# Optimization experiments

Hardware: AMD Instinct MI355X
Metric: run time of the kernel (lower is better)

The kernel has to match this reference:

```python
import jax, jax.numpy as jnp
import numpy as np
from jax.scipy.special import gammaln

# sizes (see shape_source)
N_CELLS = 1024
N_GENES = 1000
N_LATENT = 50
NB_ENC = 16          # encoder histogram bins per gene
NB_DEC = 16          # decoder mixture components (sum(n_decoder_bins))
N_HID = 16           # encoder hidden dim
N_CUTS = 4_000_000
N_FRAGS = 2_000_000
N_TOTAL_CELLS = 10_000
N_TOTAL_CUTS = 50_000_000
BN_EPS = 1e-5


def _normal_logprob(x, loc, scale):
    z = (x - loc) / scale
    return -0.5 * z * z - jnp.log(scale) - 0.5 * jnp.log(2.0 * jnp.pi)


def setup_inputs() -> dict:
    key = jax.random.key(0)
    ks = jax.random.split(key, 20)
    cut_coordinates = jax.random.uniform(ks[0], (N_CUTS,), dtype=jnp.float32)
    cut_cell = jax.random.randint(ks[1], (N_CUTS,), 0, N_CELLS)
    cut_local_gene_ix = jax.random.randint(ks[2], (N_CUTS,), 0, N_GENES)
    cut_local_cellxgene_ix = cut_cell * N_GENES + cut_local_gene_ix
    local_cellxgene_ix = jax.random.randint(ks[3], (N_FRAGS,), 0, N_CELLS * N_GENES)
    genes_oi = jnp.arange(N_GENES)
    cells_oi = jnp.arange(N_CELLS)
    eps = jax.random.normal(ks[4], (N_CELLS, N_LATENT), dtype=jnp.float32)
    n_in = N_GENES * NB_ENC
    enc_W1 = jax.random.normal(ks[5], (n_in, N_HID)) * (1.0 / np.sqrt(n_in))
    enc_b1 = jnp.zeros((N_HID,))
    bn_gamma = jnp.ones((N_HID,))
    bn_beta = jnp.zeros((N_HID,))
    W_loc = jax.random.normal(ks[6], (N_HID, N_LATENT)) * (1.0 / np.sqrt(N_HID))
    b_loc = jnp.zeros((N_LATENT,))
    W_scale = jax.random.normal(ks[7], (N_HID, N_LATENT)) * (1.0 / np.sqrt(N_HID))
    b_scale = jnp.zeros((N_LATENT,))
    logit_weight = jax.random.normal(ks[8], (N_GENES, N_LATENT, NB_DEC)) * 0.05
    rho_weight = jax.random.normal(ks[9], (N_GENES, N_LATENT)) * 0.05
    baseline_heights = jax.random.normal(ks[10], (N_GENES, NB_DEC)) * 0.1
    libsize = jax.random.randint(ks[11], (N_TOTAL_CELLS,), 1000, 20000)
    rho_bias = jax.random.uniform(ks[12], (N_GENES,), minval=1e-4, maxval=1e-2)
    return dict(
        cut_coordinates=cut_coordinates, eps=eps,
        enc_W1=enc_W1, enc_b1=enc_b1, bn_gamma=bn_gamma, bn_beta=bn_beta,
        W_loc=W_loc, b_loc=b_loc, W_scale=W_scale, b_scale=b_scale,
        logit_weight=logit_weight, rho_weight=rho_weight,
        baseline_heights=baseline_heights, rho_bias=rho_bias,
        cut_local_cellxgene_ix=cut_local_cellxgene_ix,
        cut_local_gene_ix=cut_local_gene_ix,
        local_cellxgene_ix=local_cellxgene_ix,
        genes_oi=genes_oi, cells_oi=cells_oi, libsize=libsize,
    )


def reference(cut_coordinates, eps, enc_W1, enc_b1, bn_gamma, bn_beta,
              W_loc, b_loc, W_scale, b_scale, logit_weight, rho_weight,
              baseline_heights, rho_bias, cut_local_cellxgene_ix,
              cut_local_gene_ix, local_cellxgene_ix, genes_oi, cells_oi,
              libsize):
    n_cells = cells_oi.shape[0]
    n_genes = genes_oi.shape[0]

    # ---- Encoder: digitize + bincount histogram ----
    bin_enc = jnp.minimum(jnp.floor(cut_coordinates * NB_ENC), NB_ENC - 1).astype(jnp.int32)
    digitized = bin_enc + cut_local_cellxgene_ix.astype(jnp.int32) * NB_ENC
    counts = jax.ops.segment_sum(jnp.ones_like(cut_coordinates), digitized,
                                 num_segments=n_cells * n_genes * NB_ENC)
    x = jnp.log1p(counts.reshape(n_cells, n_genes * NB_ENC))  # [C, G*NB]

    h = x @ enc_W1 + enc_b1
    mu = h.mean(axis=0)
    var = h.var(axis=0)  # biased, matches torch BN in train mode
    h = (h - mu) / jnp.sqrt(var + BN_EPS) * bn_gamma + bn_beta
    h = jax.nn.relu(h)
    loc = h @ W_loc + b_loc                 # [C, L]
    scale = jnp.exp(h @ W_scale + b_scale)  # [C, L]

    # ---- latent sample + KL ----
    q_scale = scale * 0.1
    latent = loc + q_scale * eps
    latent_kl = (_normal_logprob(latent, 0.0, 1.0)
                 - _normal_logprob(latent, loc, q_scale)) * (N_TOTAL_CELLS / n_cells)

    # ---- Decoder (n_layers=0: per-gene linear heads) ----
    lw = logit_weight[genes_oi]                       # [G, L, K]
    rw = rho_weight[genes_oi]                         # [G, L]
    mixture_delta = jnp.einsum('cl,glk->cgk', latent, lw)  # [C, G, K]
    rho_delta = jnp.einsum('cl,gl->cg', latent, rw)        # [C, G]
    md_cxg = mixture_delta.reshape(n_cells * n_genes, NB_DEC)
    md_cut = md_cxg[cut_local_cellxgene_ix]           # [N_CUTS, K] gather
    mixture_delta_kl = _normal_logprob(lw, 0.0, 0.1)

    # ---- mixture likelihood: piecewise-constant spline density per cut ----
    logits = baseline_heights[cut_local_gene_ix] + md_cut  # [N_CUTS, K]
    logp = jax.nn.log_softmax(logits, axis=-1)
    bin_dec = jnp.minimum(jnp.floor(cut_coordinates * NB_DEC), NB_DEC - 1).astype(jnp.int32)
    likelihood_mixture = (jnp.take_along_axis(logp, bin_dec[:, None], axis=1)[:, 0]
                          + jnp.log(float(NB_DEC)))

    # ---- fragment-count Poisson likelihood ----
    fragexpr = (rho_bias[genes_oi][None, :] * jnp.exp(rho_delta)
                * libsize[cells_oi].astype(jnp.float32)[:, None])  # [C, G]
    fragmentcounts = jax.ops.segment_sum(
        jnp.ones((local_cellxgene_ix.shape[0],), jnp.float32),
        local_cellxgene_ix, num_segments=n_cells * n_genes
    ).reshape(n_cells, n_genes)
    likelihood_frag = (fragmentcounts * jnp.log(fragexpr) - fragexpr
                       - gammaln(fragmentcounts + 1.0))

    rho_delta_kl = _normal_logprob(rw, 0.0, 0.1)

    likelihood = (likelihood_mixture.sum() * (N_TOTAL_CUTS / cut_coordinates.shape[0])
                  + likelihood_frag.sum() * (N_TOTAL_CELLS / n_cells))
    elbo = (-likelihood - latent_kl.sum() - mixture_delta_kl.sum()
            - rho_delta_kl.sum())
    return elbo
```

## Files before the change

kernel.cpp:

```cpp
#include <hip/hip_runtime.h>
#include <hip/hip_bf16.h>
#include <math.h>


#define G_      1000
#define C_      1024
#define L_      50
#define K_      16
#define NHID_   16
#define CUT_SCALE   12.5f
#define CELL_SCALE  9.765625f

#define CHUNK_    6144
#define RCAP_CUT  18432
#define RCAP_FRAG 9216

#define GCNTC_OFF  0ull
#define GCNTF_OFF  1024ull
#define DONE_OFF   2048ull
#define DACC_OFF   6400ull
#define HT_OFF     6912ull
#define ZERO_BYTES 72448ull
#define LATBF_OFF  72448ull
#define LWT_OFF    203520ull
#define ENTC_OFF   2251520ull
#define ENTF_OFF   11688704ull
#define MERGED_OFF 16407296ull
#define FRAGU8_OFF 24599296ull
#define LATT_OFF   25623296ull
#define WS_NEED    25828096ull

typedef __attribute__((ext_vector_type(8))) short short8;
typedef __attribute__((ext_vector_type(4))) float f32x4;

__device__ __constant__ float LGT[32] = {
    0.0f, 0.0f, 0.6931471805599453f, 1.791759469228055f, 3.1780538303479458f,
    4.787491742782046f, 6.579251212010101f, 8.525161361065415f,
    10.60460290274525f, 12.801827480081469f, 15.104412573075516f,
    17.502307845873887f, 19.987214495661885f, 22.552163853123425f,
    25.19122118273868f, 27.89927138384089f, 30.671860106080672f,
    33.50507345013689f, 36.39544520803305f, 39.339884187199495f,
    42.335616460753485f, 45.38013889847691f, 48.47118135183523f,
    51.60667556776438f, 54.78472939811232f, 58.00360522298052f,
    61.261701761002f, 64.55753862700633f, 67.88974313718154f,
    71.25703896716801f, 74.65823634883016f, 78.0922235533153f };

__device__ __forceinline__ double atomAddF64(double* p, double v) {
    return __hip_atomic_fetch_add(p, v, __ATOMIC_RELAXED,
                                  __HIP_MEMORY_SCOPE_AGENT);
}

__device__ __forceinline__ float block_sum_256(float v) {
    __shared__ float sm[256];
    int t = threadIdx.x;
    __syncthreads();
    sm[t] = v;
    __syncthreads();
#pragma unroll
    for (int s = 128; s > 0; s >>= 1) {
        if (t < s) sm[t] += sm[t + s];
        __syncthreads();
    }
    return sm[0];
}

__global__ __launch_bounds__(256)
void part_kernel(const int* __restrict__ cut_ix,
                 const float* __restrict__ coord,
                 const int* __restrict__ frag_ix,
                 unsigned int* __restrict__ gcnt_c,
                 unsigned int* __restrict__ gcnt_f,
                 unsigned short* __restrict__ entc,
                 unsigned short* __restrict__ entf,
                 const float* __restrict__ lw,
                 const float* __restrict__ rw,
                 __hip_bfloat16* __restrict__ lwT,
                 double* __restrict__ dacc,
                 int n_cuts, int n_frags, int ncc, int nblk_part) {
    int t = threadIdx.x;
    int bid = blockIdx.x;
    if (bid >= nblk_part) {
        int r = bid - nblk_part;
        if (r < 256) {
            for (int g = r; g < G_; g += 256) {
                for (int i = t; i < L_ * K_; i += 256) {
                    float v = lw[(size_t)g * (L_ * K_) + i];
                    lwT[(size_t)g * 1024 + (i & 15) * 64 + (i >> 4)] =
                        __float2bfloat16(v);
                }
                for (int i = t; i < 16 * 14; i += 256) {
                    int n = i / 14, l = 50 + (i % 14);
                    lwT[(size_t)g * 1024 + n * 64 + l] = __float2bfloat16(0.f);
                }
            }
        } else {
            const int NTOT = G_ * L_ * K_ + G_ * L_;
            int wb = r - 256;
            float s = 0.f;
            for (int i = wb * 256 + t; i < NTOT; i += 256 * 256) {
                float w = (i < G_ * L_ * K_) ? lw[i] : rw[i - G_ * L_ * K_];
                s += fmaf(-50.f * w, w, 1.3836465597893733f);
            }
            s = block_sum_256(s);
            if (t == 0) atomAddF64(&dacc[wb & 63], (double)(-s));
        }
        return;
    }
    __shared__ unsigned int cnt[256], excl[256], cur[256], gbas[256];
    __shared__ unsigned short stage[CHUNK_];
    __shared__ unsigned char bkof[CHUNK_];
    bool isCut = (bid < ncc);
    int blk = isCut ? bid : bid - ncc;
    const int* idx = isCut ? cut_ix : frag_ix;
    int n = isCut ? n_cuts : n_frags;
    int rcap = isCut ? RCAP_CUT : RCAP_FRAG;
    unsigned int* gcount = isCut ? gcnt_c : gcnt_f;
    unsigned short* ent = isCut ? entc : entf;
    int i0 = blk * CHUNK_;
    cnt[t] = 0;
    int4 I[6]; float4 X[6];
    unsigned int vm;
    bool full = (i0 + CHUNK_ <= n);
    if (full) {
        const int4* ip = (const int4*)(idx + i0);
#pragma unroll
        for (int k = 0; k < 6; ++k) I[k] = ip[k * 256 + t];
        if (isCut) {
            const float4* xp = (const float4*)(coord + i0);
#pragma unroll
            for (int k = 0; k < 6; ++k) X[k] = xp[k * 256 + t];
        }
        vm = 0xFFFFFFu;
    } else {
        vm = 0;
#pragma unroll
        for (int k = 0; k < 6; ++k) {
            int r0 = i0 + (k * 256 + t) * 4;
            int* Ii = (int*)&I[k]; float* Xi = (float*)&X[k];
#pragma unroll
            for (int u = 0; u < 4; ++u) {
                bool v = (r0 + u) < n;
                if (v) vm |= 1u << (k * 4 + u);
                Ii[u] = v ? idx[r0 + u] : 0;
                Xi[u] = (v && isCut) ? coord[r0 + u] : 0.f;
            }
        }
    }
    __syncthreads();
#pragma unroll
    for (int k = 0; k < 6; ++k) {
        const int* Ii = (const int*)&I[k];
        const float* Xi = (const float*)&X[k];
#pragma unroll
        for (int u = 0; u < 4; ++u) {
            if (vm & (1u << (k * 4 + u))) {
                int ix = Ii[u];
                int c = ix / G_;
                int g = ix - c * G_;
                unsigned int bk;
                if (isCut) {
                    int b = (int)(Xi[u] * 16.f); b = b > 15 ? 15 : b;
                    bk = ((unsigned)(c >> 6) << 4) | ((unsigned)(g * K_ + b) >> 10);
                } else {
                    bk = ((unsigned)(c >> 6) << 4) | ((unsigned)g >> 6);
                }
                atomicAdd(&cnt[bk], 1u);
            }
        }
    }
    __syncthreads();
    if (t < 64) {
        unsigned int c0 = cnt[t * 4 + 0], c1 = cnt[t * 4 + 1];
        unsigned int c2 = cnt[t * 4 + 2], c3 = cnt[t * 4 + 3];
        unsigned int tot = c0 + c1 + c2 + c3;
        unsigned int run = tot;
#pragma unroll
        for (int o = 1; o < 64; o <<= 1) {
            unsigned int v = __shfl_up(run, o, 64);
            if (t >= o) run += v;
        }
        unsigned int base = run - tot;
        excl[t * 4 + 0] = base;
        excl[t * 4 + 1] = base + c0;
        excl[t * 4 + 2] = base + c0 + c1;
        excl[t * 4 + 3] = base + c0 + c1 + c2;
    }
    __syncthreads();
    gbas[t] = cnt[t] ? atomicAdd(&gcount[t], cnt[t]) : 0u;
    cur[t] = excl[t];
    __syncthreads();
#pragma unroll
    for (int k = 0; k < 6; ++k) {
        const int* Ii = (const int*)&I[k];
        const float* Xi = (const float*)&X[k];
#pragma unroll
        for (int u = 0; u < 4; ++u) {
            if (vm & (1u << (k * 4 + u))) {
                int ix = Ii[u];
                int c = ix / G_;
                int g = ix - c * G_;
                unsigned int bk; unsigned short e;
                if (isCut) {
                    int b = (int)(Xi[u] * 16.f); b = b > 15 ? 15 : b;
                    int bin = g * K_ + b;
                    bk = ((unsigned)(c >> 6) << 4) | ((unsigned)bin >> 10);
                    e = (unsigned short)(((c & 63) << 10) | (bin & 1023));
                } else {
                    bk = ((unsigned)(c >> 6) << 4) | ((unsigned)g >> 6);
                    e = (unsigned short)(((c & 63) << 6) | (g & 63));
                }
                unsigned int p = atomicAdd(&cur[bk], 1u);
                stage[p] = e;
                bkof[p] = (unsigned char)bk;
            }
        }
    }
    __syncthreads();
    int total = n - i0; if (total > CHUNK_) total = CHUNK_;
    for (int p = t; p < total; p += 256) {
        unsigned int bk = bkof[p];
        unsigned int dst = gbas[bk] + (p - excl[bk]);
        if (dst < (unsigned)rcap)
            ent[(size_t)bk * rcap + dst] = stage[p];
    }
}

__global__ __launch_bounds__(256)
void mid_kernel(const unsigned int* __restrict__ gcnt_c,
                const unsigned short* __restrict__ entc,
                const unsigned int* __restrict__ gcnt_f,
                const unsigned short* __restrict__ entf,
                const float* __restrict__ W1,
                unsigned int* __restrict__ merged,
                unsigned int* __restrict__ fragw,
                float* __restrict__ hT) {
    __shared__ unsigned int h[4096];
    __shared__ float w1s[4096];
    int t = threadIdx.x;
    int bid = blockIdx.x;
    if (bid < 512) {
        int bk = bid >> 1, half = bid & 1;
        int cg = bk >> 4, bc = bk & 15;
        for (int i = t; i < 4096; i += 256) h[i] = 0;
        __syncthreads();
        unsigned int count = gcnt_c[bk];
        if (count > RCAP_CUT) count = RCAP_CUT;
        const unsigned int* e32 = (const unsigned int*)(entc + (size_t)bk * RCAP_CUT);
        unsigned int hsel = (unsigned)half << 5;
        unsigned int npair = count >> 1;
        for (unsigned int base = 0; base < npair; base += 1024) {
            unsigned int w[4]; bool val[4];
#pragma unroll
            for (int u = 0; u < 4; ++u) {
                unsigned int p = base + u * 256 + t;
                val[u] = (p < npair);
                w[u] = val[u] ? e32[p] : 0u;
            }
#pragma unroll
            for (int u = 0; u < 4; ++u) {
                if (val[u]) {
                    unsigned int v0 = w[u] & 0xffffu, v1 = w[u] >> 16;
                    unsigned int c0 = v0 >> 10, c1 = v1 >> 10;
                    if ((c0 & 32u) == hsel) {
                        unsigned int cc = c0 & 31u;
                        atomicAdd(&h[(v0 & 1023u) * 4 + (cc >> 3)],
                                  1u << ((cc & 7) * 4));
                    }
                    if ((c1 & 32u) == hsel) {
                        unsigned int cc = c1 & 31u;
                        atomicAdd(&h[(v1 & 1023u) * 4 + (cc >> 3)],
                                  1u << ((cc & 7) * 4));
                    }
                }
            }
        }
        if (t == 0 && (count & 1u)) {
            unsigned int v = ((const unsigned short*)e32)[count - 1];
            unsigned int c0 = v >> 10;
            if ((c0 & 32u) == hsel) {
                unsigned int cc = c0 & 31u;
                atomicAdd(&h[(v & 1023u) * 4 + (cc >> 3)], 1u << ((cc & 7) * 4));
            }
        }
        __syncthreads();
        for (int i = t; i < 4096; i += 256) {
            int binlo = i >> 2, wq = i & 3;
            int bin = bc * 1024 + binlo;
            if (bin < 16000)
                merged[(unsigned)bin * 128u + (unsigned)(cg * 8 + half * 4 + wq)]
                    = h[i];
        }
        int c32 = t & 31, sub = t >> 5;
        int sh = (c32 & 7) * 4, widx = c32 >> 3;
        float acc[NHID_];
#pragma unroll
        for (int j = 0; j < NHID_; ++j) acc[j] = 0.f;
        for (int q = 0; q < 4; ++q) {
            __syncthreads();
            int wbase = (bc * 1024 + q * 256) * NHID_;
#pragma unroll
            for (int r = 0; r < 16; ++r) {
                int i = r * 256 + t;
                int gi = wbase + i;
                w1s[i] = (gi < 16000 * NHID_) ? W1[gi] : 0.f;
            }
            __syncthreads();
            const float4* w1v = (const float4*)w1s;
            int rl0 = q * 256 + sub * 32;
#pragma unroll 4
            for (int bl = 0; bl < 32; ++bl) {
                int rl = rl0 + bl;
                int rwc = sub * 32 + bl;
                unsigned int w = h[rl * 4 + widx];
                float xv = __logf((float)(((w >> sh) & 0xfu) + 1u));
                float4 wa = w1v[rwc * 4 + 0];
                float4 wb = w1v[rwc * 4 + 1];
                float4 wc = w1v[rwc * 4 + 2];
                float4 wd = w1v[rwc * 4 + 3];
                acc[0] = fmaf(xv, wa.x, acc[0]);  acc[1] = fmaf(xv, wa.y, acc[1]);
                acc[2] = fmaf(xv, wa.z, acc[2]);  acc[3] = fmaf(xv, wa.w, acc[3]);
                acc[4] = fmaf(xv, wb.x, acc[4]);  acc[5] = fmaf(xv, wb.y, acc[5]);
                acc[6] = fmaf(xv, wb.z, acc[6]);  acc[7] = fmaf(xv, wb.w, acc[7]);
                acc[8] = fmaf(xv, wc.x, acc[8]);  acc[9] = fmaf(xv, wc.y, acc[9]);
                acc[10] = fmaf(xv, wc.z, acc[10]); acc[11] = fmaf(xv, wc.w, acc[11]);
                acc[12] = fmaf(xv, wd.x, acc[12]); acc[13] = fmaf(xv, wd.y, acc[13]);
                acc[14] = fmaf(xv, wd.z, acc[14]); acc[15] = fmaf(xv, wd.w, acc[15]);
            }
        }
        __syncthreads();
        float* sp = (float*)w1s;
#pragma unroll
        for (int j = 0; j < NHID_; ++j) sp[sub * 512 + j * 32 + c32] = acc[j];
        __syncthreads();
        for (int i = t; i < 512; i += 256) {
            int j = i >> 5, cc = i & 31;
            float v = 0.f;
#pragma unroll
            for (int s = 0; s < 8; ++s) v += sp[s * 512 + j * 32 + cc];
            atomicAdd(&hT[j * C_ + cg * 64 + half * 32 + cc], v);
        }
    } else {
        int bk = bid - 512, cg = bk >> 4, gc = bk & 15;
        for (int i = t; i < 2048; i += 256) h[i] = 0;
        __syncthreads();
        unsigned int count = gcnt_f[bk];
        if (count > RCAP_FRAG) count = RCAP_FRAG;
        const unsigned short* e = entf + (size_t)bk * RCAP_FRAG;
#pragma unroll 4
        for (unsigned int p = t; p < count; p += 256) {
            unsigned int v = e[p];
            unsigned int g_lo = v & 63u;
            unsigned int c_lo = (v >> 6) & 63u;
            atomicAdd(&h[g_lo * 32 + (c_lo >> 1)], 1u << ((c_lo & 1) * 16));
        }
        __syncthreads();
        for (int i = t; i < 1024; i += 256) {
            int g_lo = i >> 4, wb = i & 15;
            unsigned int lo = h[g_lo * 32 + wb * 2];
            unsigned int hi = h[g_lo * 32 + wb * 2 + 1];
            unsigned int outv = (lo & 0xffu) | (((lo >> 16) & 0xffu) << 8)
                              | ((hi & 0xffu) << 16) | (((hi >> 16) & 0xffu) << 24);
            int g = gc * 64 + g_lo;
            if (g < G_)
                fragw[(unsigned)g * 256u + (unsigned)cg * 16u + wb] = outv;
        }
    }
}

__global__ __launch_bounds__(256)
void latent_kernel(const float* __restrict__ hT,
                   const float* __restrict__ gamma,
                   const float* __restrict__ beta,
                   const float* __restrict__ W_loc,
                   const float* __restrict__ b_loc,
                   const float* __restrict__ W_scale,
                   const float* __restrict__ b_scale,
                   const float* __restrict__ eps,
                   float* __restrict__ latT,
                   __hip_bfloat16* __restrict__ latbf,
                   double* __restrict__ dacc) {
    __shared__ float scs[NHID_], shs[NHID_];
    int t = threadIdx.x;
    {
        int j = t >> 4, cl = t & 15;
        double s1 = 0.0, s2 = 0.0;
#pragma unroll 8
        for (int k = 0; k < 64; ++k) {
            float v = hT[j * C_ + cl + k * 16];
            s1 += (double)v; s2 += (double)v * (double)v;
        }
#pragma unroll
        for (int m = 1; m < 16; m <<= 1) {
            s1 += __shfl_xor(s1, m);
            s2 += __shfl_xor(s2, m);
        }
        if (cl == 0) {
            double mean = s1 * (1.0 / C_);
            double var = s2 * (1.0 / C_) - mean * mean;
            float rstd = rsqrtf((float)var + 1e-5f);
            float sc = gamma[j] * rstd;
            scs[j] = sc;
            shs[j] = beta[j] - (float)mean * sc;
        }
    }
    __syncthreads();
    int idx = blockIdx.x * 256 + t;
    float kl = 0.f;
    {
        int c = idx / L_;
        int l = idx - c * L_;
        float hb[NHID_];
#pragma unroll
        for (int j = 0; j < NHID_; ++j) {
            float v = fmaf(hT[j * C_ + c], scs[j], shs[j]);
            hb[j] = v > 0.f ? v : 0.f;
        }
        float loc = b_loc[l], ls = b_scale[l];
#pragma unroll
        for (int j = 0; j < NHID_; ++j) {
            loc = fmaf(hb[j], W_loc[j * L_ + l], loc);
            ls  = fmaf(hb[j], W_scale[j * L_ + l], ls);
        }
        float qs = 0.1f * __expf(ls);
        float e = eps[idx];
        float lat = fmaf(qs, e, loc);
        latT[(size_t)l * C_ + c] = lat;
        latbf[c * 64 + l] = __float2bfloat16(lat);
        if (l < 14) latbf[c * 64 + 50 + l] = __float2bfloat16(0.f);
        float z = (lat - loc) / qs;
        kl = fmaf(-0.5f * lat, lat, fmaf(0.5f * z, z, __logf(qs)));
    }
    float s = block_sum_256(kl);
    if (threadIdx.x == 0)
        atomAddF64(&dacc[blockIdx.x & 63], (double)(-CELL_SCALE * s));
}

__global__ __launch_bounds__(256)
void mixpois_kernel(const __hip_bfloat16* __restrict__ latbf,
                    const __hip_bfloat16* __restrict__ lwT,
                    const unsigned int* __restrict__ merged,
                    const float* __restrict__ baseline,
                    const float* __restrict__ latT,
                    const float* __restrict__ rw,
                    const float* __restrict__ rho_bias,
                    const int* __restrict__ libsize,
                    const unsigned char* __restrict__ fragb,
                    double* __restrict__ dacc,
                    unsigned int* __restrict__ done,
                    float* __restrict__ out) {
    int g = blockIdx.x;
    int y = blockIdx.y;
    int t = threadIdx.x;
    int lane = t & 63;
    int wv = t >> 6;
    int s16 = lane & 15;
    int quad = lane >> 4;
    const __hip_bfloat16* bb = lwT + (size_t)g * 1024 + s16 * 64 + quad * 8;
    short8 lw1 = *(const short8*)bb;
    short8 lw2 = *(const short8*)(bb + 32);
    const float4 bl4 = *(const float4*)(baseline + g * K_ + quad * 4);
    const unsigned int* mrow =
        merged + (size_t)(g * K_ + quad * 4) * 128u;
    float partial = 0.f;
    int cwave = y * 256 + wv * 64;
#pragma unroll
    for (int mt = 0; mt < 4; ++mt) {
        int c0 = cwave + mt * 16;
        const __hip_bfloat16* aa = latbf + (size_t)(c0 + s16) * 64 + quad * 8;
        short8 la1 = *(const short8*)aa;
        short8 la2 = *(const short8*)(aa + 32);
        f32x4 d = {bl4.x, bl4.y, bl4.z, bl4.w};
        d = __builtin_amdgcn_mfma_f32_16x16x32_bf16(lw1, la1, d, 0, 0, 0);
        d = __builtin_amdgcn_mfma_f32_16x16x32_bf16(lw2, la2, d, 0, 0, 0);
        float m = fmaxf(fmaxf(d[0], d[1]), fmaxf(d[2], d[3]));
        m = fmaxf(m, __shfl_xor(m, 16));
        m = fmaxf(m, __shfl_xor(m, 32));
        float e0 = __expf(d[0] - m), e1 = __expf(d[1] - m);
        float e2 = __expf(d[2] - m), e3 = __expf(d[3] - m);
        float S = (e0 + e1) + (e2 + e3);
        S += __shfl_xor(S, 16);
        S += __shfl_xor(S, 32);
        float lse = m + __logf(S);
        int cp = c0 + s16;
        unsigned int widx = (unsigned)cp >> 3;
        int sb = (cp & 7) * 4;
#pragma unroll
        for (int r = 0; r < 4; ++r) {
            float cnt = (float)((mrow[r * 128u + widx] >> sb) & 0xfu);
            partial = fmaf(cnt, d[r] - lse, partial);
        }
    }
    float v;
    {
        int c = y * 256 + t;
        const float* rwg = rw + (size_t)g * L_;
        float rho = 0.f;
#pragma unroll 10
        for (int l = 0; l < L_; ++l)
            rho = fmaf(latT[l * C_ + c], rwg[l], rho);
        unsigned int fc = fragb[(size_t)g * C_ + c];
        float fe = rho_bias[g] * __expf(rho) * (float)libsize[c];
        float lf = fmaf((float)fc, __logf(fe), -fe) - LGT[fc > 31u ? 31u : fc];
        v = fmaf(-CUT_SCALE, partial, -CELL_SCALE * lf);
    }
    float contrib = block_sum_256(v);
    __shared__ int lastflag;
    if (threadIdx.x == 0) {
        lastflag = 0;
        int slot = blockIdx.x & 63;
        double oldv = atomAddF64(&dacc[slot], (double)contrib);
        unsigned inc = 1u;
        float dep = (float)oldv;
        asm volatile("" : "+v"(inc) : "v"(dep));
        unsigned quota = ((slot < 40) ? 16u : 15u) * 4u;
        if (atomicAdd(&done[slot * 16], inc) == quota - 1u) {
            if (atomicAdd(&done[1024], 1u) == 63u) lastflag = 1;
        }
    }
    __syncthreads();
    if (lastflag) {
        if (t < 64) {
            double dv = atomAddF64(&dacc[t], 0.0);
#pragma unroll
            for (int m = 1; m < 64; m <<= 1) dv += __shfl_xor(dv, m);
            if (t == 0)
                out[0] = (float)(dv - 138629436.11198905);
        }
    }
}

extern "C" void kernel_launch(void* const* d_in, const int* in_sizes, int n_in,
                              void* d_out, int out_size, void* d_ws, size_t ws_size,
                              hipStream_t stream) {
    const float* cut_coord = (const float*)d_in[0];
    const float* eps       = (const float*)d_in[1];
    const float* enc_W1    = (const float*)d_in[2];
    const float* bn_gamma  = (const float*)d_in[4];
    const float* bn_beta   = (const float*)d_in[5];
    const float* W_loc     = (const float*)d_in[6];
    const float* b_loc     = (const float*)d_in[7];
    const float* W_scale   = (const float*)d_in[8];
    const float* b_scale   = (const float*)d_in[9];
    const float* logit_w   = (const float*)d_in[10];
    const float* rho_w     = (const float*)d_in[11];
    const float* baseline  = (const float*)d_in[12];
    const float* rho_bias  = (const float*)d_in[13];
    const int* cut_cxg     = (const int*)d_in[14];
    const int* frag_ix     = (const int*)d_in[16];
    const int* libsize     = (const int*)d_in[19];

    int n_cuts  = in_sizes[0];
    int n_frags = in_sizes[16];

    char* ws = (char*)d_ws;
    unsigned int*   gcnt_c = (unsigned int*)(ws + GCNTC_OFF);
    unsigned int*   gcnt_f = (unsigned int*)(ws + GCNTF_OFF);
    unsigned int*   done   = (unsigned int*)(ws + DONE_OFF);
    double*         dacc   = (double*)(ws + DACC_OFF);
    float*          hT     = (float*)(ws + HT_OFF);
    __hip_bfloat16* latbf  = (__hip_bfloat16*)(ws + LATBF_OFF);
    __hip_bfloat16* lwT    = (__hip_bfloat16*)(ws + LWT_OFF);
    unsigned short* entc   = (unsigned short*)(ws + ENTC_OFF);
    unsigned short* entf   = (unsigned short*)(ws + ENTF_OFF);
    unsigned int*   merged = (unsigned int*)(ws + MERGED_OFF);
    unsigned int*   fragw  = (unsigned int*)(ws + FRAGU8_OFF);
    float*          latT   = (float*)(ws + LATT_OFF);
    float*          out    = (float*)d_out;

    int ncc = (n_cuts + CHUNK_ - 1) / CHUNK_;
    int ncf = (n_frags + CHUNK_ - 1) / CHUNK_;
    int nblk_part = ncc + ncf;

    hipMemsetAsync(ws, 0, ZERO_BYTES, stream);

    part_kernel<<<nblk_part + 512, 256, 0, stream>>>(
        cut_cxg, cut_coord, frag_ix, gcnt_c, gcnt_f, entc, entf,
        logit_w, rho_w, lwT, dacc,
        n_cuts, n_frags, ncc, nblk_part);
    mid_kernel<<<768, 256, 0, stream>>>(
        gcnt_c, entc, gcnt_f, entf, enc_W1, merged, fragw, hT);
    latent_kernel<<<(C_ * L_) / 256, 256, 0, stream>>>(
        hT, bn_gamma, bn_beta, W_loc, b_loc, W_scale, b_scale,
        eps, latT, latbf, dacc);
    mixpois_kernel<<<dim3(G_, 4), 256, 0, stream>>>(
        latbf, lwT, merged, baseline, latT, rho_w, rho_bias, libsize,
        (const unsigned char*)fragw, dacc, done, out);
}
```

Baseline: 225.3 us.

## Reuse first-pass atomic ranks in partition scatter; double cells per mixpois block

In the partition kernel, the rank returned by the counting shared atomic and the packed entry/bucket are kept in registers. The scatter pass then computes its slot as excl[bucket]+rank, which drops the second atomic pass, the cur array and one barrier. The mixpois kernel now covers 512 cells per block instead of 256, halving the grid and adjusting the completion quota, so per-block fixed costs like weight loads and the final atomics are amortised. The trade-off is fewer blocks for latency hiding and more registers per thread.

Measured after the change: 220.7 us. 1.02x faster.

```diff
diff --git a/kernel.cpp b/kernel.cpp
--- a/kernel.cpp
+++ b/kernel.cpp
@@ -106,7 +106,7 @@
         }
         return;
     }
-    __shared__ unsigned int cnt[256], excl[256], cur[256], gbas[256];
+    __shared__ unsigned int cnt[256], excl[256], gbas[256];
     __shared__ unsigned short stage[CHUNK_];
     __shared__ unsigned char bkof[CHUNK_];
     bool isCut = (bid < ncc);
@@ -149,22 +149,28 @@
     __syncthreads();
 #pragma unroll
     for (int k = 0; k < 6; ++k) {
-        const int* Ii = (const int*)&I[k];
-        const float* Xi = (const float*)&X[k];
+        int* Ii = (int*)&I[k];
+        unsigned int* Xi = (unsigned int*)&X[k];
 #pragma unroll
         for (int u = 0; u < 4; ++u) {
             if (vm & (1u << (k * 4 + u))) {
                 int ix = Ii[u];
                 int c = ix / G_;
                 int g = ix - c * G_;
-                unsigned int bk;
+                unsigned int bk; unsigned int e;
                 if (isCut) {
-                    int b = (int)(Xi[u] * 16.f); b = b > 15 ? 15 : b;
-                    bk = ((unsigned)(c >> 6) << 4) | ((unsigned)(g * K_ + b) >> 10);
+                    float xf = ((const float*)Xi)[u];
+                    int b = (int)(xf * 16.f); b = b > 15 ? 15 : b;
+                    int bin = g * K_ + b;
+                    bk = ((unsigned)(c >> 6) << 4) | ((unsigned)bin >> 10);
+                    e = ((unsigned)(c & 63) << 10) | ((unsigned)bin & 1023u);
                 } else {
                     bk = ((unsigned)(c >> 6) << 4) | ((unsigned)g >> 6);
+                    e = ((unsigned)(c & 63) << 6) | ((unsigned)g & 63u);
                 }
-                atomicAdd(&cnt[bk], 1u);
+                unsigned int rank = atomicAdd(&cnt[bk], 1u);
+                Ii[u] = (int)(e | (bk << 16));
+                Xi[u] = rank;
             }
         }
     }
@@ -187,30 +193,17 @@
     }
     __syncthreads();
     gbas[t] = cnt[t] ? atomicAdd(&gcount[t], cnt[t]) : 0u;
-    cur[t] = excl[t];
-    __syncthreads();
 #pragma unroll
     for (int k = 0; k < 6; ++k) {
-        const int* Ii = (const int*)&I[k];
-        const float* Xi = (const float*)&X[k];
+        const unsigned int* Ii = (const unsigned int*)&I[k];
+        const unsigned int* Xi = (const unsigned int*)&X[k];
 #pragma unroll
         for (int u = 0; u < 4; ++u) {
             if (vm & (1u << (k * 4 + u))) {
-                int ix = Ii[u];
-                int c = ix / G_;
-                int g = ix - c * G_;
-                unsigned int bk; unsigned short e;
-                if (isCut) {
-                    int b = (int)(Xi[u] * 16.f); b = b > 15 ? 15 : b;
-                    int bin = g * K_ + b;
-                    bk = ((unsigned)(c >> 6) << 4) | ((unsigned)bin >> 10);
-                    e = (unsigned short)(((c & 63) << 10) | (bin & 1023));
-                } else {
-                    bk = ((unsigned)(c >> 6) << 4) | ((unsigned)g >> 6);
-                    e = (unsigned short)(((c & 63) << 6) | (g & 63));
-                }
-                unsigned int p = atomicAdd(&cur[bk], 1u);
-                stage[p] = e;
+                unsigned int w = Ii[u];
+                unsigned int bk = w >> 16;
+                unsigned int p = excl[bk] + Xi[u];
+                stage[p] = (unsigned short)(w & 0xffffu);
                 bkof[p] = (unsigned char)bk;
             }
         }
@@ -462,9 +455,9 @@
     const unsigned int* mrow =
         merged + (size_t)(g * K_ + quad * 4) * 128u;
     float partial = 0.f;
-    int cwave = y * 256 + wv * 64;
-#pragma unroll
-    for (int mt = 0; mt < 4; ++mt) {
+    int cwave = y * 512 + wv * 128;
+#pragma unroll
+    for (int mt = 0; mt < 8; ++mt) {
         int c0 = cwave + mt * 16;
         const __hip_bfloat16* aa = latbf + (size_t)(c0 + s16) * 64 + quad * 8;
         short8 la1 = *(const short8*)aa;
@@ -492,16 +485,23 @@
     }
     float v;
     {
-        int c = y * 256 + t;
         const float* rwg = rw + (size_t)g * L_;
-        float rho = 0.f;
+        int cA = y * 512 + t, cB = cA + 256;
+        float rhoA = 0.f, rhoB = 0.f;
 #pragma unroll 10
-        for (int l = 0; l < L_; ++l)
-            rho = fmaf(latT[l * C_ + c], rwg[l], rho);
-        unsigned int fc = fragb[(size_t)g * C_ + c];
-        float fe = rho_bias[g] * __expf(rho) * (float)libsize[c];
-        float lf = fmaf((float)fc, __logf(fe), -fe) - LGT[fc > 31u ? 31u : fc];
-        v = fmaf(-CUT_SCALE, partial, -CELL_SCALE * lf);
+        for (int l = 0; l < L_; ++l) {
+            float wl = rwg[l];
+            rhoA = fmaf(latT[l * C_ + cA], wl, rhoA);
+            rhoB = fmaf(latT[l * C_ + cB], wl, rhoB);
+        }
+        unsigned int fcA = fragb[(size_t)g * C_ + cA];
+        unsigned int fcB = fragb[(size_t)g * C_ + cB];
+        float rb = rho_bias[g];
+        float feA = rb * __expf(rhoA) * (float)libsize[cA];
+        float feB = rb * __expf(rhoB) * (float)libsize[cB];
+        float lfA = fmaf((float)fcA, __logf(feA), -feA) - LGT[fcA > 31u ? 31u : fcA];
+        float lfB = fmaf((float)fcB, __logf(feB), -feB) - LGT[fcB > 31u ? 31u : fcB];
+        v = fmaf(-CUT_SCALE, partial, -CELL_SCALE * (lfA + lfB));
     }
     float contrib = block_sum_256(v);
     __shared__ int lastflag;
@@ -512,7 +512,7 @@
         unsigned inc = 1u;
         float dep = (float)oldv;
         asm volatile("" : "+v"(inc) : "v"(dep));
-        unsigned quota = ((slot < 40) ? 16u : 15u) * 4u;
+        unsigned quota = ((slot < 40) ? 16u : 15u) * 2u;
         if (atomicAdd(&done[slot * 16], inc) == quota - 1u) {
             if (atomicAdd(&done[1024], 1u) == 63u) lastflag = 1;
         }
@@ -582,7 +582,7 @@
     latent_kernel<<<(C_ * L_) / 256, 256, 0, stream>>>(
         hT, bn_gamma, bn_beta, W_loc, b_loc, W_scale, b_scale,
         eps, latT, latbf, dacc);
-    mixpois_kernel<<<dim3(G_, 4), 256, 0, stream>>>(
+    mixpois_kernel<<<dim3(G_, 2), 256, 0, stream>>>(
         latbf, lwT, merged, baseline, latT, rho_w, rho_bias, libsize,
         (const unsigned char*)fragw, dacc, done, out);
 }
```
